# Kernel optimization log

Hardware: AMD Instinct MI355X
Metric: run time of the kernel (lower is better)

## Reference

```python
import jax, jax.numpy as jnp
import numpy as np

N = 100000      # nodes
E = 1600000     # edges
R = 4           # relations
F = 128         # node feature dim
EMB = 128       # embedding size
HID = 256       # hidden size
B = 1024        # number of (nest, food) queries


def setup_inputs() -> dict:
    key = jax.random.key(0)
    ks = jax.random.split(key, 12)
    s1 = 1.0 / np.sqrt(F)
    s2 = 1.0 / np.sqrt(EMB)
    sf = 1.0 / np.sqrt(2 * EMB)
    return {
        "x": jax.random.normal(ks[0], (N, F), jnp.float32),
        "edge_index": jax.random.randint(ks[1], (2, E), 0, N),
        "edge_type": jax.random.randint(ks[2], (E,), 0, R),
        "nest_idx": jax.random.randint(ks[3], (B,), 0, N),
        "food_idx": jax.random.randint(ks[4], (B,), 0, N),
        "W_rel1": jax.random.normal(ks[5], (R, F, EMB), jnp.float32) * s1,
        "W_root1": jax.random.normal(ks[6], (F, EMB), jnp.float32) * s1,
        "b1": jnp.zeros((EMB,), jnp.float32),
        "W_rel2": jax.random.normal(ks[7], (R, EMB, EMB), jnp.float32) * s2,
        "W_root2": jax.random.normal(ks[8], (EMB, EMB), jnp.float32) * s2,
        "b2": jnp.zeros((EMB,), jnp.float32),
        "W_fc": jax.random.normal(ks[9], (2 * EMB, HID), jnp.float32) * sf,
        "b_fc": jnp.zeros((HID,), jnp.float32),
    }


def rgcn_conv(x, src, dst, etype, W_rel, W_root, b):
    # Per-relation transform of all nodes: [N, R, O]
    h = jnp.einsum('nf,rfo->nro', x, W_rel)
    msgs = h[src, etype]                      # [E, O] gather per edge
    # Mean aggregation per (dst, relation), PyG RGCNConv default
    key = dst * R + etype                     # [E]
    deg = jax.ops.segment_sum(jnp.ones((E,), x.dtype), key, num_segments=N * R)
    norm = 1.0 / jnp.maximum(deg, 1.0)
    out = jax.ops.segment_sum(msgs * norm[key][:, None], dst, num_segments=N)
    return out + x @ W_root + b


def reference(x, edge_index, edge_type, nest_idx, food_idx,
              W_rel1, W_root1, b1, W_rel2, W_root2, b2, W_fc, b_fc):
    src, dst = edge_index[0], edge_index[1]
    h = jax.nn.relu(rgcn_conv(x, src, dst, edge_type, W_rel1, W_root1, b1))
    h = rgcn_conv(h, src, dst, edge_type, W_rel2, W_root2, b2)
    combined = jnp.concatenate([h[nest_idx], h[food_idx]], axis=-1)  # [B, 2*EMB]
    return jax.nn.relu(combined @ W_fc + b_fc)                        # [B, HID]
```

## Files before the change

### kernel.cpp

```cpp
#include <hip/hip_runtime.h>
#include <stdint.h>

#define NN 100000
#define NE 1600000
#define NR 4
#define FD 128
#define KA 512
#define KT 640
#define NQ 1024
#define HIDN 256

#define MPAD 100096
#define NBE ((NE + 2047) / 2048)
#define NCHB ((NN + 255) / 256)
#define MAXS 49152
#define NCH1 (MAXS / 256)
#define MAXL2 65536

using u16 = unsigned short;
using u32 = unsigned int;
using u8 = unsigned char;
typedef __attribute__((ext_vector_type(8))) __bf16 bf16x8;
typedef __attribute__((ext_vector_type(4))) float f32x4;

__device__ __forceinline__ u16 f2b(float f) {
    u32 u = __builtin_bit_cast(u32, f);
    u32 r = u + 0x7FFFu + ((u >> 16) & 1u);
    return (u16)(r >> 16);
}
__device__ __forceinline__ float b2f_lo(u32 v) { return __builtin_bit_cast(float, v << 16); }
__device__ __forceinline__ float b2f_hi(u32 v) { return __builtin_bit_cast(float, v & 0xFFFF0000u); }
__device__ __forceinline__ u32 pack2(float a, float b) {
    return (u32)f2b(a) | ((u32)f2b(b) << 16);
}
__device__ __forceinline__ void gload_lds16(const void* g, void* l) {
    __builtin_amdgcn_global_load_lds((const __attribute__((address_space(1))) u32*)g,
                                     (__attribute__((address_space(3))) u32*)l, 16, 0, 0);
}

__global__ __launch_bounds__(256) void mark_T(const int* __restrict__ nest,
                                              const int* __restrict__ food,
                                              u8* __restrict__ bmT, u8* __restrict__ bmS) {
    int i = blockIdx.x * 256 + threadIdx.x;
    if (i < NQ)          { int q = nest[i];      bmT[q] = 1; bmS[q] = 1; }
    else if (i < 2 * NQ) { int q = food[i - NQ]; bmT[q] = 1; bmS[q] = 1; }
}

__global__ __launch_bounds__(256) void filter_l2(const int* __restrict__ ei,
                                                 const int* __restrict__ et,
                                                 const u8* __restrict__ bmT,
                                                 u8* __restrict__ bmS,
                                                 int* __restrict__ cnts,
                                                 u32* __restrict__ l2a,
                                                 u32* __restrict__ l2d) {
    __shared__ int lcnt, lbase;
    __shared__ u32 ba[2048], bd[2048];
    int t = threadIdx.x;
    if (t == 0) lcnt = 0;
    __syncthreads();
    int e0 = blockIdx.x * 2048;
    for (int j = 0; j < 8; ++j) {
        int e = e0 + j * 256 + t;
        if (e < NE) {
            int dst = ei[NE + e];
            if (bmT[dst]) {
                int src = ei[e];
                int r = et[e];
                int pos = atomicAdd(&lcnt, 1);
                ba[pos] = (u32)src | ((u32)r << 17);
                bd[pos] = (u32)dst;
                bmS[src] = 1;
            }
        }
    }
    __syncthreads();
    if (t == 0) lbase = atomicAdd(&cnts[2], lcnt);
    __syncthreads();
    for (int i = t; i < lcnt; i += 256) {
        l2a[lbase + i] = ba[i];
        l2d[lbase + i] = bd[i];
    }
}

__global__ __launch_bounds__(256) void bm_chunk(const u8* __restrict__ bmS,
                                                const u8* __restrict__ bmT,
                                                int* __restrict__ cS, int* __restrict__ cT) {
    __shared__ int sS[256], sT[256];
    int b = blockIdx.x, t = threadIdx.x;
    int n = b * 256 + t;
    int vs = (n < NN) ? bmS[n] : 0;
    int vt = (n < NN) ? bmT[n] : 0;
    sS[t] = vs; sT[t] = vt;
    __syncthreads();
    for (int o = 128; o > 0; o >>= 1) {
        if (t < o) { sS[t] += sS[t + o]; sT[t] += sT[t + o]; }
        __syncthreads();
    }
    if (t == 0) { cS[b] = sS[0]; cT[b] = sT[0]; }
}

__global__ __launch_bounds__(512) void bm_scan(const int* __restrict__ cS,
                                               const int* __restrict__ cT,
                                               int* __restrict__ oS, int* __restrict__ oT,
                                               int* __restrict__ cnts) {
    __shared__ int sS[512], sT[512];
    int t = threadIdx.x;
    int vs = (t < NCHB) ? cS[t] : 0;
    int vt = (t < NCHB) ? cT[t] : 0;
    sS[t] = vs; sT[t] = vt;
    __syncthreads();
    for (int o = 1; o < 512; o <<= 1) {
        int a = (t >= o) ? sS[t - o] : 0;
        int c = (t >= o) ? sT[t - o] : 0;
        __syncthreads();
        sS[t] += a; sT[t] += c;
        __syncthreads();
    }
    if (t < NCHB) { oS[t] = sS[t] - vs; oT[t] = sT[t] - vt; }
    if (t == NCHB - 1) { cnts[0] = sS[t]; cnts[1] = sT[t]; }
}

__global__ __launch_bounds__(256) void bm_write(const u8* __restrict__ bmS,
                                                const u8* __restrict__ bmT,
                                                const int* __restrict__ oS,
                                                const int* __restrict__ oT,
                                                int* __restrict__ sid, int* __restrict__ tidm,
                                                int* __restrict__ snode) {
    __shared__ int sS[256], sT[256];
    int b = blockIdx.x, t = threadIdx.x;
    int n = b * 256 + t;
    int vs = (n < NN) ? bmS[n] : 0;
    int vt = (n < NN) ? bmT[n] : 0;
    sS[t] = vs; sT[t] = vt;
    __syncthreads();
    for (int o = 1; o < 256; o <<= 1) {
        int a = (t >= o) ? sS[t - o] : 0;
        int c = (t >= o) ? sT[t - o] : 0;
        __syncthreads();
        sS[t] += a; sT[t] += c;
        __syncthreads();
    }
    if (n < NN) {
        int is = oS[b] + sS[t] - vs;
        int it = oT[b] + sT[t] - vt;
        sid[n] = is;
        tidm[n] = it;
        if (vs) snode[is] = n;
    }
}

__global__ __launch_bounds__(256) void l2_count(const int* __restrict__ cnts,
                                                const u32* __restrict__ l2a,
                                                const u32* __restrict__ l2d,
                                                const int* __restrict__ tidm,
                                                int* __restrict__ deg2) {
    int n = cnts[2];
    for (int i = blockIdx.x * 256 + threadIdx.x; i < n; i += gridDim.x * 256)
        atomicAdd(&deg2[tidm[l2d[i]] * 4 + ((l2a[i] >> 17) & 3)], 1);
}

__global__ __launch_bounds__(1024) void l2_scan(const int* __restrict__ deg2,
                                                int* __restrict__ offs2,
                                                int* __restrict__ cur2) {
    __shared__ int sm[1024];
    int t = threadIdx.x;
    int v[8];
    int s = 0;
    for (int j = 0; j < 8; ++j) { v[j] = deg2[t * 8 + j]; s += v[j]; }
    sm[t] = s;
    __syncthreads();
    for (int o = 1; o < 1024; o <<= 1) {
        int n = (t >= o) ? sm[t - o] : 0;
        __syncthreads();
        sm[t] += n;
        __syncthreads();
    }
    int ex = sm[t] - s;
    for (int j = 0; j < 8; ++j) { offs2[t * 8 + j] = ex; cur2[t * 8 + j] = ex; ex += v[j]; }
    if (t == 1023) offs2[8192] = ex;
}

__global__ __launch_bounds__(256) void l2_scatter(const int* __restrict__ cnts,
                                                  const u32* __restrict__ l2a,
                                                  const u32* __restrict__ l2d,
                                                  const int* __restrict__ tidm,
                                                  const int* __restrict__ sid,
                                                  int* __restrict__ cur2,
                                                  int* __restrict__ spack2) {
    int n = cnts[2];
    for (int i = blockIdx.x * 256 + threadIdx.x; i < n; i += gridDim.x * 256) {
        u32 a = l2a[i];
        int k = tidm[l2d[i]] * 4 + ((a >> 17) & 3);
        int pos = atomicAdd(&cur2[k], 1);
        spack2[pos] = sid[a & 0x1FFFFu];
    }
}

__global__ __launch_bounds__(256) void l1_count(const int* __restrict__ ei,
                                                const int* __restrict__ et,
                                                const u8* __restrict__ bmS,
                                                const int* __restrict__ sid,
                                                int* __restrict__ deg1) {
    int e0 = blockIdx.x * 2048;
    int t = threadIdx.x;
    for (int j = 0; j < 8; ++j) {
        int e = e0 + j * 256 + t;
        if (e < NE) {
            int dst = ei[NE + e];
            if (bmS[dst]) atomicAdd(&deg1[sid[dst] * 4 + et[e]], 1);
        }
    }
}

__global__ __launch_bounds__(256) void l1_chunk(const int* __restrict__ deg1,
                                                int* __restrict__ c1) {
    __shared__ int sm[256];
    int b = blockIdx.x, t = threadIdx.x;
    int n = b * 256 + t;
    int s = deg1[4 * n] + deg1[4 * n + 1] + deg1[4 * n + 2] + deg1[4 * n + 3];
    sm[t] = (s + 7) & ~7;
    __syncthreads();
    for (int o = 128; o > 0; o >>= 1) {
        if (t < o) sm[t] += sm[t + o];
        __syncthreads();
    }
    if (t == 0) c1[b] = sm[0];
}

__global__ __launch_bounds__(256) void l1_scan(const int* __restrict__ c1,
                                               int* __restrict__ o1) {
    __shared__ int sm[256];
    int t = threadIdx.x;
    int v = (t < NCH1) ? c1[t] : 0;
    sm[t] = v;
    __syncthreads();
    for (int o = 1; o < 256; o <<= 1) {
        int n = (t >= o) ? sm[t - o] : 0;
        __syncthreads();
        sm[t] += n;
        __syncthreads();
    }
    if (t < NCH1) o1[t] = sm[t] - v;
}

__global__ __launch_bounds__(256) void l1_write(const int* __restrict__ deg1,
                                                const int* __restrict__ o1,
                                                int* __restrict__ offs6s,
                                                int* __restrict__ cur1,
                                                int* __restrict__ spack1) {
    __shared__ int sm[256];
    int b = blockIdx.x, t = threadIdx.x;
    int n = b * 256 + t;
    int d0 = deg1[4 * n], d1 = deg1[4 * n + 1], d2 = deg1[4 * n + 2], d3 = deg1[4 * n + 3];
    int s = d0 + d1 + d2 + d3;
    int sp = (s + 7) & ~7;
    sm[t] = sp;
    __syncthreads();
    for (int o = 1; o < 256; o <<= 1) {
        int v = (t >= o) ? sm[t - o] : 0;
        __syncthreads();
        sm[t] += v;
        __syncthreads();
    }
    int e0 = o1[b] + sm[t] - sp;
    int e1 = e0 + d0, e2 = e1 + d1, e3 = e2 + d2, e4 = e3 + d3, eL = e0 + sp;
    int* o6 = offs6s + (size_t)n * 6;
    o6[0] = e0; o6[1] = e1; o6[2] = e2; o6[3] = e3; o6[4] = e4; o6[5] = eL;
    cur1[4 * n] = e0; cur1[4 * n + 1] = e1; cur1[4 * n + 2] = e2; cur1[4 * n + 3] = e3;
    for (int i = e4; i < eL; ++i) spack1[i] = NN;
}

__global__ __launch_bounds__(256) void l1_scatter(const int* __restrict__ ei,
                                                  const int* __restrict__ et,
                                                  const u8* __restrict__ bmS,
                                                  const int* __restrict__ sid,
                                                  int* __restrict__ cur1,
                                                  int* __restrict__ spack1) {
    int e0 = blockIdx.x * 2048;
    int t = threadIdx.x;
    for (int j = 0; j < 8; ++j) {
        int e = e0 + j * 256 + t;
        if (e < NE) {
            int dst = ei[NE + e];
            if (bmS[dst]) {
                int pos = atomicAdd(&cur1[sid[dst] * 4 + et[e]], 1);
                spack1[pos] = ei[e];
            }
        }
    }
}

__global__ __launch_bounds__(256) void cvt_bf16(const float* __restrict__ in,
                                                u16* __restrict__ outp, int n) {
    int i = blockIdx.x * 256 + threadIdx.x;
    int idx = i * 4;
    if (idx >= n) return;
    float4 v = *(const float4*)(in + idx);
    u32 lo = (u32)f2b(v.x) | ((u32)f2b(v.y) << 16);
    u32 hi = (u32)f2b(v.z) | ((u32)f2b(v.w) << 16);
    *(uint2*)(outp + idx) = make_uint2(lo, hi);
}

__global__ __launch_bounds__(256) void prep_B(const float* __restrict__ Wrel,
                                              const float* __restrict__ Wroot,
                                              u16* __restrict__ Bt) {
    int i = blockIdx.x * 256 + threadIdx.x;
    if (i >= FD * KT) return;
    int k = i % KT;
    int o = i / KT;
    float v = (k < 512) ? Wrel[(size_t)k * FD + o] : Wroot[(size_t)(k - 512) * FD + o];
    Bt[i] = f2b(v);
}

__global__ __launch_bounds__(256) void agg_s(const int* __restrict__ cnts,
                                             const int* __restrict__ offs6s,
                                             const int* __restrict__ spack1,
                                             const u32* __restrict__ fp,
                                             u16* __restrict__ Aout) {
    int wid = threadIdx.x >> 6, lane = threadIdx.x & 63;
    int row = blockIdx.x * 4 + wid;
    if (row >= cnts[0]) return;

    const int* ob = offs6s + (size_t)row * 6;
    int o0 = __builtin_amdgcn_readfirstlane(ob[0]);
    int o1 = __builtin_amdgcn_readfirstlane(ob[1]);
    int o2 = __builtin_amdgcn_readfirstlane(ob[2]);
    int o3 = __builtin_amdgcn_readfirstlane(ob[3]);
    int o4 = __builtin_amdgcn_readfirstlane(ob[4]);
    int oL = __builtin_amdgcn_readfirstlane(ob[5]);

    float a00 = 0, a01 = 0, a10 = 0, a11 = 0, a20 = 0, a21 = 0, a30 = 0, a31 = 0;

    for (int e = o0; e < oL; e += 8) {
        int p[8];
        u32 v[8];
#pragma unroll
        for (int j = 0; j < 8; ++j)
            p[j] = __builtin_amdgcn_readfirstlane(spack1[e + j]);
#pragma unroll
        for (int j = 0; j < 8; ++j) v[j] = fp[(size_t)p[j] * 64 + lane];
#pragma unroll
        for (int j = 0; j < 8; ++j) {
            int ij = e + j;
            float f0 = b2f_lo(v[j]);
            float f1 = b2f_hi(v[j]);
            if (ij < o1)      { a00 += f0; a01 += f1; }
            else if (ij < o2) { a10 += f0; a11 += f1; }
            else if (ij < o3) { a20 += f0; a21 += f1; }
            else              { a30 += f0; a31 += f1; }
        }
    }

    int d0 = o1 - o0, d1 = o2 - o1, d2 = o3 - o2, d3 = o4 - o3;
    float s0 = 1.0f / (float)(d0 > 1 ? d0 : 1);
    float s1 = 1.0f / (float)(d1 > 1 ? d1 : 1);
    float s2 = 1.0f / (float)(d2 > 1 ? d2 : 1);
    float s3 = 1.0f / (float)(d3 > 1 ? d3 : 1);
    u16* Ao = Aout + (size_t)row * KA + lane * 2;
    __builtin_nontemporal_store(pack2(a00 * s0, a01 * s0), (u32*)(Ao + 0));
    __builtin_nontemporal_store(pack2(a10 * s1, a11 * s1), (u32*)(Ao + 128));
    __builtin_nontemporal_store(pack2(a20 * s2, a21 * s2), (u32*)(Ao + 256));
    __builtin_nontemporal_store(pack2(a30 * s3, a31 * s3), (u32*)(Ao + 384));
}

__global__ __launch_bounds__(256) void agg_q2(const int* __restrict__ offs2,
                                              const int* __restrict__ spack2,
                                              const u32* __restrict__ h1s4,
                                              const int* __restrict__ nest,
                                              const int* __restrict__ food,
                                              const int* __restrict__ tidm,
                                              const int* __restrict__ sid,
                                              u16* __restrict__ Aout,
                                              int* __restrict__ sidq) {
    int wid = threadIdx.x >> 6, lane = threadIdx.x & 63;
    int row = blockIdx.x * 4 + wid;
    if (row >= 2 * NQ) return;
    int q = (row < NQ) ? nest[row] : food[row - NQ];
    q = __builtin_amdgcn_readfirstlane(q);
    int tq = __builtin_amdgcn_readfirstlane(tidm[q]);
    if (lane == 0) sidq[row] = sid[q];
    const int* ob = offs2 + (size_t)tq * 4;
    int o[5];
#pragma unroll
    for (int i = 0; i < 5; ++i) o[i] = __builtin_amdgcn_readfirstlane(ob[i]);
    u16* Ao = Aout + (size_t)row * KA + lane * 2;
#pragma unroll
    for (int r = 0; r < 4; ++r) {
        int s = o[r], t = o[r + 1], last = t - 1;
        float a0 = 0, a1 = 0;
        for (int e = s; e < t; e += 8) {
            int p[8];
            u32 v[8];
#pragma unroll
            for (int j = 0; j < 8; ++j) {
                int ij = e + j;
                int cl = ij <= last ? ij : last;
                int pv = __builtin_amdgcn_readfirstlane(spack2[cl]);
                p[j] = (ij <= last) ? pv : MAXS;
            }
#pragma unroll
            for (int j = 0; j < 8; ++j) v[j] = h1s4[(size_t)p[j] * 64 + lane];
#pragma unroll
            for (int j = 0; j < 8; ++j) { a0 += b2f_lo(v[j]); a1 += b2f_hi(v[j]); }
        }
        int d = t - s;
        float sc = 1.0f / (float)(d > 1 ? d : 1);
        *(u32*)(Ao + r * 128) = pack2(a0 * sc, a1 * sc);
    }
}

__global__ __launch_bounds__(256) void gemm_lds3(const u16* __restrict__ A,
                                                 const u16* __restrict__ rootSrc,
                                                 const int* __restrict__ rootIdx,
                                                 const u16* __restrict__ Bt,
                                                 const float* __restrict__ bias,
                                                 void* __restrict__ Cout,
                                                 const int* __restrict__ Mptr, int Mstatic,
                                                 int relu, int outBf16) {
    int M = Mptr ? Mptr[0] : Mstatic;
    int row0 = blockIdx.x * 128;
    if (row0 >= M) return;
    __shared__ u16 As[3][8192];
    int tid = threadIdx.x;
    int wid = tid >> 6, lane = tid & 63;
    int wm = wid >> 1, wn = wid & 1;
    int lr = lane & 15, hi = lane >> 4;

    f32x4 acc[4][4];
#pragma unroll
    for (int i = 0; i < 4; ++i)
#pragma unroll
        for (int j = 0; j < 4; ++j) acc[i][j] = (f32x4){0.f, 0.f, 0.f, 0.f};

    int srow = wid * 8 + (lane >> 3);
    int sg = (lane & 7) ^ ((lane >> 3) & 7);

    auto stage = [&](int t, int buf) {
#pragma unroll
        for (int i = 0; i < 4; ++i) {
            int r = i * 32 + srow;
            int gr = row0 + r;
            const u16* src;
            if (t < 8) {
                src = A + (size_t)gr * KA + t * 64 + sg * 8;
            } else {
                int idx = rootIdx ? rootIdx[gr] : gr;
                if ((u32)idx > (u32)NN) idx = 0;
                src = rootSrc + (size_t)idx * FD + (t - 8) * 64 + sg * 8;
            }
            gload_lds16(src, (char*)As[buf] + i * 4096 + wid * 1024);
        }
    };

    stage(0, 0);
    stage(1, 1);

    for (int t = 0; t < 10; ++t) {
        int cur = t % 3;
        bf16x8 bfr[2][4];
#pragma unroll
        for (int kk = 0; kk < 2; ++kk)
#pragma unroll
            for (int ni = 0; ni < 4; ++ni) {
                int col = wn * 64 + ni * 16 + lr;
                bfr[kk][ni] = *reinterpret_cast<const bf16x8*>(
                    Bt + (size_t)col * KT + t * 64 + kk * 32 + hi * 8);
            }
        bool staged = (t + 2 < 10);
        if (staged) stage(t + 2, (t + 2) % 3);
        if (staged) asm volatile("s_waitcnt vmcnt(4)" ::: "memory");
        else        asm volatile("s_waitcnt vmcnt(0)" ::: "memory");
        __builtin_amdgcn_s_barrier();
        __builtin_amdgcn_sched_barrier(0);
#pragma unroll
        for (int kk = 0; kk < 2; ++kk) {
            bf16x8 afr[4];
#pragma unroll
            for (int mi = 0; mi < 4; ++mi) {
                int r = wm * 64 + mi * 16 + lr;
                int sp = (kk * 4 + hi) ^ (r & 7);
                afr[mi] = *reinterpret_cast<const bf16x8*>((char*)As[cur] + r * 128 + sp * 16);
            }
#pragma unroll
            for (int mi = 0; mi < 4; ++mi)
#pragma unroll
                for (int ni = 0; ni < 4; ++ni)
                    acc[mi][ni] = __builtin_amdgcn_mfma_f32_16x16x32_bf16(afr[mi], bfr[kk][ni], acc[mi][ni], 0, 0, 0);
        }
        asm volatile("s_waitcnt lgkmcnt(0)" ::: "memory");
        __builtin_amdgcn_s_barrier();
    }

#pragma unroll
    for (int mi = 0; mi < 4; ++mi)
#pragma unroll
        for (int ni = 0; ni < 4; ++ni) {
            int col = wn * 64 + ni * 16 + lr;
            float bv = bias[col];
#pragma unroll
            for (int rg = 0; rg < 4; ++rg) {
                int row = row0 + wm * 64 + mi * 16 + hi * 4 + rg;
                if (row < M) {
                    float v = acc[mi][ni][rg] + bv;
                    if (relu) v = fmaxf(v, 0.f);
                    if (outBf16) ((u16*)Cout)[(size_t)row * FD + col] = f2b(v);
                    else ((float*)Cout)[(size_t)row * FD + col] = v;
                }
            }
        }
}

__global__ __launch_bounds__(256) void fc_kernel(const float* __restrict__ h2q,
                                                 const float* __restrict__ Wfc,
                                                 const float* __restrict__ bfc,
                                                 float* __restrict__ out) {
    __shared__ float comb[2 * FD];
    int q = blockIdx.x, t = threadIdx.x;
    if (t < FD) comb[t] = h2q[(size_t)q * FD + t];
    else comb[t] = h2q[(size_t)(NQ + q) * FD + (t - FD)];
    __syncthreads();
    float s = bfc[t];
#pragma unroll 4
    for (int k = 0; k < 2 * FD; ++k) s += comb[k] * Wfc[(size_t)k * HIDN + t];
    out[(size_t)q * HIDN + t] = fmaxf(s, 0.f);
}

extern "C" void kernel_launch(void* const* d_in, const int* in_sizes, int n_in,
                              void* d_out, int out_size, void* d_ws, size_t ws_size,
                              hipStream_t stream) {
    const float* x      = (const float*)d_in[0];
    const int*   ei     = (const int*)d_in[1];
    const int*   et     = (const int*)d_in[2];
    const int*   nest   = (const int*)d_in[3];
    const int*   food   = (const int*)d_in[4];
    const float* Wrel1  = (const float*)d_in[5];
    const float* Wroot1 = (const float*)d_in[6];
    const float* b1     = (const float*)d_in[7];
    const float* Wrel2  = (const float*)d_in[8];
    const float* Wroot2 = (const float*)d_in[9];
    const float* b2     = (const float*)d_in[10];
    const float* Wfc    = (const float*)d_in[11];
    const float* bfc    = (const float*)d_in[12];
    float* out = (float*)d_out;

    char* w = (char*)d_ws;
    size_t off = 0;
    auto take = [&](size_t b) {
        char* p = w + off;
        off += b;
        off = (off + 255) & ~(size_t)255;
        return p;
    };
    size_t zero0 = off;
    int* cnts   = (int*)take(256);
    u8* bmT     = (u8*)take(NN);
    u8* bmS     = (u8*)take(NN);
    int* deg2   = (int*)take(8192 * 4);
    int* deg1   = (int*)take((size_t)4 * MAXS * 4);
    int* snode  = (int*)take((size_t)MAXS * 4);
    size_t zeroSz = off - zero0;
    char* zbase = w + zero0;
    int* oS     = (int*)take((size_t)NCHB * 4);
    int* oT     = (int*)take((size_t)NCHB * 4);
    int* c1     = (int*)take((size_t)NCH1 * 4);
    int* o1     = (int*)take((size_t)NCH1 * 4);
    int* sid    = (int*)take((size_t)NN * 4);
    int* tidm   = (int*)take((size_t)NN * 4);
    u32* l2a    = (u32*)take((size_t)MAXL2 * 4);
    u32* l2d    = (u32*)take((size_t)MAXL2 * 4);
    int* offs2  = (int*)take((size_t)8193 * 4);
    int* cur2   = (int*)take((size_t)8192 * 4);
    int* spack2 = (int*)take((size_t)MAXL2 * 4);
    int* offs6s = (int*)take((size_t)MAXS * 6 * 4);
    int* cur1   = (int*)take((size_t)4 * MAXS * 4);
    int* spack1 = (int*)take(((size_t)NE + 8 * MAXS) * 4);
    int* sidq   = (int*)take((size_t)2 * NQ * 4);
    u16* xh     = (u16*)take((size_t)MPAD * FD * 2);
    u16* Bt1    = (u16*)take((size_t)FD * KT * 2);
    u16* Bt2    = (u16*)take((size_t)FD * KT * 2);
    u16* A1s    = (u16*)take((size_t)MAXS * KA * 2);
    u16* h1s    = (u16*)take(((size_t)MAXS + 1) * FD * 2);
    u16* A2     = (u16*)take((size_t)2 * NQ * KA * 2);
    float* h2q  = (float*)take((size_t)2 * NQ * FD * 4);

    hipMemsetAsync(zbase, 0, zeroSz, stream);
    hipMemsetAsync(xh + (size_t)NN * FD, 0, FD * 2, stream);
    hipMemsetAsync(h1s + (size_t)MAXS * FD, 0, FD * 2, stream);

    cvt_bf16<<<((NN * FD / 4) + 255) / 256, 256, 0, stream>>>(x, xh, NN * FD);
    prep_B<<<(FD * KT + 255) / 256, 256, 0, stream>>>(Wrel1, Wroot1, Bt1);
    prep_B<<<(FD * KT + 255) / 256, 256, 0, stream>>>(Wrel2, Wroot2, Bt2);

    mark_T<<<(2 * NQ + 255) / 256, 256, 0, stream>>>(nest, food, bmT, bmS);
    filter_l2<<<NBE, 256, 0, stream>>>(ei, et, bmT, bmS, cnts, l2a, l2d);
    bm_chunk<<<NCHB, 256, 0, stream>>>(bmS, bmT, oS, oT);
    bm_scan<<<1, 512, 0, stream>>>(oS, oT, oS, oT, cnts);
    bm_write<<<NCHB, 256, 0, stream>>>(bmS, bmT, oS, oT, sid, tidm, snode);

    l2_count<<<128, 256, 0, stream>>>(cnts, l2a, l2d, tidm, deg2);
    l2_scan<<<1, 1024, 0, stream>>>(deg2, offs2, cur2);
    l2_scatter<<<128, 256, 0, stream>>>(cnts, l2a, l2d, tidm, sid, cur2, spack2);

    l1_count<<<NBE, 256, 0, stream>>>(ei, et, bmS, sid, deg1);
    l1_chunk<<<NCH1, 256, 0, stream>>>(deg1, c1);
    l1_scan<<<1, 256, 0, stream>>>(c1, o1);
    l1_write<<<NCH1, 256, 0, stream>>>(deg1, o1, offs6s, cur1, spack1);
    l1_scatter<<<NBE, 256, 0, stream>>>(ei, et, bmS, sid, cur1, spack1);

    agg_s<<<MAXS / 4, 256, 0, stream>>>(cnts, offs6s, spack1, (const u32*)xh, A1s);
    gemm_lds3<<<MAXS / 128, 256, 0, stream>>>(A1s, xh, snode, Bt1, b1,
                                              (void*)h1s, cnts, 0, 1, 1);

    agg_q2<<<(2 * NQ + 3) / 4, 256, 0, stream>>>(offs2, spack2, (const u32*)h1s,
                                                 nest, food, tidm, sid, A2, sidq);
    gemm_lds3<<<(2 * NQ) / 128, 256, 0, stream>>>(A2, h1s, sidq, Bt2, b2,
                                                  (void*)h2q, nullptr, 2 * NQ, 0, 0);
    fc_kernel<<<NQ, 256, 0, stream>>>(h2q, Wfc, bfc, out);
}
```

Measured before the change: 229.5 us.

## Replace scan-based compaction with atomic allocation and fuse prep kernels

Merges the bf16 conversion, the weight transposes and the query marking into one launch. It replaces the multi-kernel prefix-scan compactions (bitmap chunk/scan/write, the layer-2 count/scan and the layer-1 chunk/scan/write) with single-pass atomic-counter allocation. Layer-2 degrees are now counted directly in filter_l2 and indexed by node id, which drops the target-id map. This removes about eight kernel launches and their serial dependencies. In exchange the node order and CSR offsets become nondeterministic, and a larger per-node degree array (NN×4 ints) must be zeroed in the memset.

```diff
diff --git a/kernel.cpp b/kernel.cpp
--- a/kernel.cpp
+++ b/kernel.cpp
@@ -10,12 +10,12 @@
 #define NQ 1024
 #define HIDN 256
 
-#define MPAD 100096
 #define NBE ((NE + 2047) / 2048)
 #define NCHB ((NN + 255) / 256)
 #define MAXS 49152
 #define NCH1 (MAXS / 256)
 #define MAXL2 65536
+#define CVTB 12500
 
 using u16 = unsigned short;
 using u32 = unsigned int;
@@ -38,12 +38,43 @@
                                      (__attribute__((address_space(3))) u32*)l, 16, 0, 0);
 }
 
-__global__ __launch_bounds__(256) void mark_T(const int* __restrict__ nest,
-                                              const int* __restrict__ food,
-                                              u8* __restrict__ bmT, u8* __restrict__ bmS) {
-    int i = blockIdx.x * 256 + threadIdx.x;
-    if (i < NQ)          { int q = nest[i];      bmT[q] = 1; bmS[q] = 1; }
-    else if (i < 2 * NQ) { int q = food[i - NQ]; bmT[q] = 1; bmS[q] = 1; }
+__global__ __launch_bounds__(256) void prep_all(const float* __restrict__ x,
+                                                u16* __restrict__ xh,
+                                                const float* __restrict__ Wrel1,
+                                                const float* __restrict__ Wroot1,
+                                                u16* __restrict__ Bt1,
+                                                const float* __restrict__ Wrel2,
+                                                const float* __restrict__ Wroot2,
+                                                u16* __restrict__ Bt2,
+                                                const int* __restrict__ nest,
+                                                const int* __restrict__ food,
+                                                u8* __restrict__ bmT,
+                                                u8* __restrict__ bmS) {
+    int b = blockIdx.x, t = threadIdx.x;
+    if (b < CVTB) {
+        int idx = (b * 256 + t) * 4;
+        if (idx < NN * FD) {
+            float4 v = *(const float4*)(x + idx);
+            u32 lo = (u32)f2b(v.x) | ((u32)f2b(v.y) << 16);
+            u32 hi = (u32)f2b(v.z) | ((u32)f2b(v.w) << 16);
+            *(uint2*)(xh + idx) = make_uint2(lo, hi);
+        }
+    } else if (b < CVTB + 640) {
+        int rel2 = (b >= CVTB + 320);
+        int i = (b - CVTB - rel2 * 320) * 256 + t;
+        if (i < FD * KT) {
+            int k = i % KT;
+            int o = i / KT;
+            const float* Wr = rel2 ? Wrel2 : Wrel1;
+            const float* Wo = rel2 ? Wroot2 : Wroot1;
+            float v = (k < 512) ? Wr[(size_t)k * FD + o] : Wo[(size_t)(k - 512) * FD + o];
+            (rel2 ? Bt2 : Bt1)[i] = f2b(v);
+        }
+    } else {
+        int i = (b - CVTB - 640) * 256 + t;
+        if (i < NQ)          { int q = nest[i];      bmT[q] = 1; bmS[q] = 1; }
+        else if (i < 2 * NQ) { int q = food[i - NQ]; bmT[q] = 1; bmS[q] = 1; }
+    }
 }
 
 __global__ __launch_bounds__(256) void filter_l2(const int* __restrict__ ei,
@@ -51,6 +82,7 @@
                                                  const u8* __restrict__ bmT,
                                                  u8* __restrict__ bmS,
                                                  int* __restrict__ cnts,
+                                                 int* __restrict__ deg2n,
                                                  u32* __restrict__ l2a,
                                                  u32* __restrict__ l2d) {
     __shared__ int lcnt, lbase;
@@ -70,6 +102,7 @@
                 ba[pos] = (u32)src | ((u32)r << 17);
                 bd[pos] = (u32)dst;
                 bmS[src] = 1;
+                atomicAdd(&deg2n[dst * 4 + r], 1);
             }
         }
     }
@@ -82,116 +115,44 @@
     }
 }
 
-__global__ __launch_bounds__(256) void bm_chunk(const u8* __restrict__ bmS,
-                                                const u8* __restrict__ bmT,
-                                                int* __restrict__ cS, int* __restrict__ cT) {
-    __shared__ int sS[256], sT[256];
-    int b = blockIdx.x, t = threadIdx.x;
-    int n = b * 256 + t;
-    int vs = (n < NN) ? bmS[n] : 0;
-    int vt = (n < NN) ? bmT[n] : 0;
-    sS[t] = vs; sT[t] = vt;
-    __syncthreads();
-    for (int o = 128; o > 0; o >>= 1) {
-        if (t < o) { sS[t] += sS[t + o]; sT[t] += sT[t + o]; }
-        __syncthreads();
-    }
-    if (t == 0) { cS[b] = sS[0]; cT[b] = sT[0]; }
-}
-
-__global__ __launch_bounds__(512) void bm_scan(const int* __restrict__ cS,
-                                               const int* __restrict__ cT,
-                                               int* __restrict__ oS, int* __restrict__ oT,
-                                               int* __restrict__ cnts) {
-    __shared__ int sS[512], sT[512];
-    int t = threadIdx.x;
-    int vs = (t < NCHB) ? cS[t] : 0;
-    int vt = (t < NCHB) ? cT[t] : 0;
-    sS[t] = vs; sT[t] = vt;
-    __syncthreads();
-    for (int o = 1; o < 512; o <<= 1) {
-        int a = (t >= o) ? sS[t - o] : 0;
-        int c = (t >= o) ? sT[t - o] : 0;
-        __syncthreads();
-        sS[t] += a; sT[t] += c;
-        __syncthreads();
-    }
-    if (t < NCHB) { oS[t] = sS[t] - vs; oT[t] = sT[t] - vt; }
-    if (t == NCHB - 1) { cnts[0] = sS[t]; cnts[1] = sT[t]; }
-}
-
-__global__ __launch_bounds__(256) void bm_write(const u8* __restrict__ bmS,
-                                                const u8* __restrict__ bmT,
-                                                const int* __restrict__ oS,
-                                                const int* __restrict__ oT,
-                                                int* __restrict__ sid, int* __restrict__ tidm,
-                                                int* __restrict__ snode) {
-    __shared__ int sS[256], sT[256];
-    int b = blockIdx.x, t = threadIdx.x;
-    int n = b * 256 + t;
-    int vs = (n < NN) ? bmS[n] : 0;
-    int vt = (n < NN) ? bmT[n] : 0;
-    sS[t] = vs; sT[t] = vt;
-    __syncthreads();
-    for (int o = 1; o < 256; o <<= 1) {
-        int a = (t >= o) ? sS[t - o] : 0;
-        int c = (t >= o) ? sT[t - o] : 0;
-        __syncthreads();
-        sS[t] += a; sT[t] += c;
-        __syncthreads();
-    }
-    if (n < NN) {
-        int is = oS[b] + sS[t] - vs;
-        int it = oT[b] + sT[t] - vt;
+__global__ __launch_bounds__(256) void bm_compact(const u8* __restrict__ bmS,
+                                                  int* __restrict__ cnts,
+                                                  int* __restrict__ sid,
+                                                  int* __restrict__ snode) {
+    int n = blockIdx.x * 256 + threadIdx.x;
+    if (n < NN && bmS[n]) {
+        int is = atomicAdd(&cnts[0], 1);
         sid[n] = is;
-        tidm[n] = it;
-        if (vs) snode[is] = n;
-    }
-}
-
-__global__ __launch_bounds__(256) void l2_count(const int* __restrict__ cnts,
-                                                const u32* __restrict__ l2a,
-                                                const u32* __restrict__ l2d,
-                                                const int* __restrict__ tidm,
-                                                int* __restrict__ deg2) {
-    int n = cnts[2];
-    for (int i = blockIdx.x * 256 + threadIdx.x; i < n; i += gridDim.x * 256)
-        atomicAdd(&deg2[tidm[l2d[i]] * 4 + ((l2a[i] >> 17) & 3)], 1);
-}
-
-__global__ __launch_bounds__(1024) void l2_scan(const int* __restrict__ deg2,
-                                                int* __restrict__ offs2,
-                                                int* __restrict__ cur2) {
-    __shared__ int sm[1024];
-    int t = threadIdx.x;
-    int v[8];
-    int s = 0;
-    for (int j = 0; j < 8; ++j) { v[j] = deg2[t * 8 + j]; s += v[j]; }
-    sm[t] = s;
-    __syncthreads();
-    for (int o = 1; o < 1024; o <<= 1) {
-        int n = (t >= o) ? sm[t - o] : 0;
-        __syncthreads();
-        sm[t] += n;
-        __syncthreads();
-    }
-    int ex = sm[t] - s;
-    for (int j = 0; j < 8; ++j) { offs2[t * 8 + j] = ex; cur2[t * 8 + j] = ex; ex += v[j]; }
-    if (t == 1023) offs2[8192] = ex;
+        snode[is] = n;
+    }
+}
+
+__global__ __launch_bounds__(256) void l2_offs(const int* __restrict__ deg2n,
+                                               int* __restrict__ cnts,
+                                               int* __restrict__ offs2n,
+                                               int* __restrict__ cur2n) {
+    int n = blockIdx.x * 256 + threadIdx.x;
+    if (n >= NN) return;
+    int d0 = deg2n[n * 4], d1 = deg2n[n * 4 + 1], d2 = deg2n[n * 4 + 2], d3 = deg2n[n * 4 + 3];
+    int s = d0 + d1 + d2 + d3;
+    if (s == 0) return;
+    int base = atomicAdd(&cnts[3], s);
+    int e0 = base, e1 = e0 + d0, e2 = e1 + d1, e3 = e2 + d2;
+    offs2n[n * 4] = e0; offs2n[n * 4 + 1] = e1; offs2n[n * 4 + 2] = e2; offs2n[n * 4 + 3] = e3;
+    cur2n[n * 4] = e0;  cur2n[n * 4 + 1] = e1;  cur2n[n * 4 + 2] = e2;  cur2n[n * 4 + 3] = e3;
 }
 
 __global__ __launch_bounds__(256) void l2_scatter(const int* __restrict__ cnts,
                                                   const u32* __restrict__ l2a,
                                                   const u32* __restrict__ l2d,
-                                                  const int* __restrict__ tidm,
                                                   const int* __restrict__ sid,
-                                                  int* __restrict__ cur2,
+                                                  int* __restrict__ cur2n,
                                                   int* __restrict__ spack2) {
     int n = cnts[2];
     for (int i = blockIdx.x * 256 + threadIdx.x; i < n; i += gridDim.x * 256) {
         u32 a = l2a[i];
-        int k = tidm[l2d[i]] * 4 + ((a >> 17) & 3);
-        int pos = atomicAdd(&cur2[k], 1);
+        int k = (int)l2d[i] * 4 + (int)((a >> 17) & 3);
+        int pos = atomicAdd(&cur2n[k], 1);
         spack2[pos] = sid[a & 0x1FFFFu];
     }
 }
@@ -212,58 +173,18 @@
     }
 }
 
-__global__ __launch_bounds__(256) void l1_chunk(const int* __restrict__ deg1,
-                                                int* __restrict__ c1) {
-    __shared__ int sm[256];
-    int b = blockIdx.x, t = threadIdx.x;
-    int n = b * 256 + t;
-    int s = deg1[4 * n] + deg1[4 * n + 1] + deg1[4 * n + 2] + deg1[4 * n + 3];
-    sm[t] = (s + 7) & ~7;
-    __syncthreads();
-    for (int o = 128; o > 0; o >>= 1) {
-        if (t < o) sm[t] += sm[t + o];
-        __syncthreads();
-    }
-    if (t == 0) c1[b] = sm[0];
-}
-
-__global__ __launch_bounds__(256) void l1_scan(const int* __restrict__ c1,
-                                               int* __restrict__ o1) {
-    __shared__ int sm[256];
-    int t = threadIdx.x;
-    int v = (t < NCH1) ? c1[t] : 0;
-    sm[t] = v;
-    __syncthreads();
-    for (int o = 1; o < 256; o <<= 1) {
-        int n = (t >= o) ? sm[t - o] : 0;
-        __syncthreads();
-        sm[t] += n;
-        __syncthreads();
-    }
-    if (t < NCH1) o1[t] = sm[t] - v;
-}
-
-__global__ __launch_bounds__(256) void l1_write(const int* __restrict__ deg1,
-                                                const int* __restrict__ o1,
-                                                int* __restrict__ offs6s,
-                                                int* __restrict__ cur1,
-                                                int* __restrict__ spack1) {
-    __shared__ int sm[256];
-    int b = blockIdx.x, t = threadIdx.x;
-    int n = b * 256 + t;
+__global__ __launch_bounds__(256) void l1_offs(const int* __restrict__ deg1,
+                                               int* __restrict__ cnts,
+                                               int* __restrict__ offs6s,
+                                               int* __restrict__ cur1,
+                                               int* __restrict__ spack1) {
+    int n = blockIdx.x * 256 + threadIdx.x;
+    if (n >= MAXS) return;
     int d0 = deg1[4 * n], d1 = deg1[4 * n + 1], d2 = deg1[4 * n + 2], d3 = deg1[4 * n + 3];
     int s = d0 + d1 + d2 + d3;
     int sp = (s + 7) & ~7;
-    sm[t] = sp;
-    __syncthreads();
-    for (int o = 1; o < 256; o <<= 1) {
-        int v = (t >= o) ? sm[t - o] : 0;
-        __syncthreads();
-        sm[t] += v;
-        __syncthreads();
-    }
-    int e0 = o1[b] + sm[t] - sp;
-    int e1 = e0 + d0, e2 = e1 + d1, e3 = e2 + d2, e4 = e3 + d3, eL = e0 + sp;
+    int base = sp ? atomicAdd(&cnts[4], sp) : 0;
+    int e0 = base, e1 = e0 + d0, e2 = e1 + d1, e3 = e2 + d2, e4 = e3 + d3, eL = base + sp;
     int* o6 = offs6s + (size_t)n * 6;
     o6[0] = e0; o6[1] = e1; o6[2] = e2; o6[3] = e3; o6[4] = e4; o6[5] = eL;
     cur1[4 * n] = e0; cur1[4 * n + 1] = e1; cur1[4 * n + 2] = e2; cur1[4 * n + 3] = e3;
@@ -290,28 +211,6 @@
     }
 }
 
-__global__ __launch_bounds__(256) void cvt_bf16(const float* __restrict__ in,
-                                                u16* __restrict__ outp, int n) {
-    int i = blockIdx.x * 256 + threadIdx.x;
-    int idx = i * 4;
-    if (idx >= n) return;
-    float4 v = *(const float4*)(in + idx);
-    u32 lo = (u32)f2b(v.x) | ((u32)f2b(v.y) << 16);
-    u32 hi = (u32)f2b(v.z) | ((u32)f2b(v.w) << 16);
-    *(uint2*)(outp + idx) = make_uint2(lo, hi);
-}
-
-__global__ __launch_bounds__(256) void prep_B(const float* __restrict__ Wrel,
-                                              const float* __restrict__ Wroot,
-                                              u16* __restrict__ Bt) {
-    int i = blockIdx.x * 256 + threadIdx.x;
-    if (i >= FD * KT) return;
-    int k = i % KT;
-    int o = i / KT;
-    float v = (k < 512) ? Wrel[(size_t)k * FD + o] : Wroot[(size_t)(k - 512) * FD + o];
-    Bt[i] = f2b(v);
-}
-
 __global__ __launch_bounds__(256) void agg_s(const int* __restrict__ cnts,
                                              const int* __restrict__ offs6s,
                                              const int* __restrict__ spack1,
@@ -363,12 +262,12 @@
     __builtin_nontemporal_store(pack2(a30 * s3, a31 * s3), (u32*)(Ao + 384));
 }
 
-__global__ __launch_bounds__(256) void agg_q2(const int* __restrict__ offs2,
+__global__ __launch_bounds__(256) void agg_q2(const int* __restrict__ offs2n,
+                                              const int* __restrict__ deg2n,
                                               const int* __restrict__ spack2,
                                               const u32* __restrict__ h1s4,
                                               const int* __restrict__ nest,
                                               const int* __restrict__ food,
-                                              const int* __restrict__ tidm,
                                               const int* __restrict__ sid,
                                               u16* __restrict__ Aout,
                                               int* __restrict__ sidq) {
@@ -377,16 +276,13 @@
     if (row >= 2 * NQ) return;
     int q = (row < NQ) ? nest[row] : food[row - NQ];
     q = __builtin_amdgcn_readfirstlane(q);
-    int tq = __builtin_amdgcn_readfirstlane(tidm[q]);
     if (lane == 0) sidq[row] = sid[q];
-    const int* ob = offs2 + (size_t)tq * 4;
-    int o[5];
-#pragma unroll
-    for (int i = 0; i < 5; ++i) o[i] = __builtin_amdgcn_readfirstlane(ob[i]);
     u16* Ao = Aout + (size_t)row * KA + lane * 2;
 #pragma unroll
     for (int r = 0; r < 4; ++r) {
-        int s = o[r], t = o[r + 1], last = t - 1;
+        int s = __builtin_amdgcn_readfirstlane(offs2n[q * 4 + r]);
+        int d = __builtin_amdgcn_readfirstlane(deg2n[q * 4 + r]);
+        int t = s + d, last = t - 1;
         float a0 = 0, a1 = 0;
         for (int e = s; e < t; e += 8) {
             int p[8];
@@ -403,7 +299,6 @@
 #pragma unroll
             for (int j = 0; j < 8; ++j) { a0 += b2f_lo(v[j]); a1 += b2f_hi(v[j]); }
         }
-        int d = t - s;
         float sc = 1.0f / (float)(d > 1 ? d : 1);
         *(u32*)(Ao + r * 128) = pack2(a0 * sc, a1 * sc);
     }
@@ -551,68 +446,52 @@
         off = (off + 255) & ~(size_t)255;
         return p;
     };
+    u16* xh     = (u16*)take((size_t)NN * FD * 2);
     size_t zero0 = off;
+    take(FD * 2);
     int* cnts   = (int*)take(256);
     u8* bmT     = (u8*)take(NN);
     u8* bmS     = (u8*)take(NN);
-    int* deg2   = (int*)take(8192 * 4);
+    int* deg2n  = (int*)take((size_t)NN * 4 * 4);
     int* deg1   = (int*)take((size_t)4 * MAXS * 4);
     int* snode  = (int*)take((size_t)MAXS * 4);
+    u16* h1s    = (u16*)take(((size_t)MAXS + 1) * FD * 2);
     size_t zeroSz = off - zero0;
     char* zbase = w + zero0;
-    int* oS     = (int*)take((size_t)NCHB * 4);
-    int* oT     = (int*)take((size_t)NCHB * 4);
-    int* c1     = (int*)take((size_t)NCH1 * 4);
-    int* o1     = (int*)take((size_t)NCH1 * 4);
     int* sid    = (int*)take((size_t)NN * 4);
-    int* tidm   = (int*)take((size_t)NN * 4);
     u32* l2a    = (u32*)take((size_t)MAXL2 * 4);
     u32* l2d    = (u32*)take((size_t)MAXL2 * 4);
-    int* offs2  = (int*)take((size_t)8193 * 4);
-    int* cur2   = (int*)take((size_t)8192 * 4);
+    int* offs2n = (int*)take((size_t)NN * 4 * 4);
+    int* cur2n  = (int*)take((size_t)NN * 4 * 4);
     int* spack2 = (int*)take((size_t)MAXL2 * 4);
     int* offs6s = (int*)take((size_t)MAXS * 6 * 4);
     int* cur1   = (int*)take((size_t)4 * MAXS * 4);
     int* spack1 = (int*)take(((size_t)NE + 8 * MAXS) * 4);
     int* sidq   = (int*)take((size_t)2 * NQ * 4);
-    u16* xh     = (u16*)take((size_t)MPAD * FD * 2);
     u16* Bt1    = (u16*)take((size_t)FD * KT * 2);
     u16* Bt2    = (u16*)take((size_t)FD * KT * 2);
     u16* A1s    = (u16*)take((size_t)MAXS * KA * 2);
-    u16* h1s    = (u16*)take(((size_t)MAXS + 1) * FD * 2);
     u16* A2     = (u16*)take((size_t)2 * NQ * KA * 2);
     float* h2q  = (float*)take((size_t)2 * NQ * FD * 4);
 
     hipMemsetAsync(zbase, 0, zeroSz, stream);
-    hipMemsetAsync(xh + (size_t)NN * FD, 0, FD * 2, stream);
-    hipMemsetAsync(h1s + (size_t)MAXS * FD, 0, FD * 2, stream);
-
-    cvt_bf16<<<((NN * FD / 4) + 255) / 256, 256, 0, stream>>>(x, xh, NN * FD);
-    prep_B<<<(FD * KT + 255) / 256, 256, 0, stream>>>(Wrel1, Wroot1, Bt1);
-    prep_B<<<(FD * KT + 255) / 256, 256, 0, stream>>>(Wrel2, Wroot2, Bt2);
-
-    mark_T<<<(2 * NQ + 255) / 256, 256, 0, stream>>>(nest, food, bmT, bmS);
-    filter_l2<<<NBE, 256, 0, stream>>>(ei, et, bmT, bmS, cnts, l2a, l2d);
-    bm_chunk<<<NCHB, 256, 0, stream>>>(bmS, bmT, oS, oT);
-    bm_scan<<<1, 512, 0, stream>>>(oS, oT, oS, oT, cnts);
-    bm_write<<<NCHB, 256, 0, stream>>>(bmS, bmT, oS, oT, sid, tidm, snode);
-
-    l2_count<<<128, 256, 0, stream>>>(cnts, l2a, l2d, tidm, deg2);
-    l2_scan<<<1, 1024, 0, stream>>>(deg2, offs2, cur2);
-    l2_scatter<<<128, 256, 0, stream>>>(cnts, l2a, l2d, tidm, sid, cur2, spack2);
-
+
+    prep_all<<<CVTB + 640 + 8, 256, 0, stream>>>(x, xh, Wrel1, Wroot1, Bt1,
+                                                 Wrel2, Wroot2, Bt2, nest, food, bmT, bmS);
+    filter_l2<<<NBE, 256, 0, stream>>>(ei, et, bmT, bmS, cnts, deg2n, l2a, l2d);
+    bm_compact<<<NCHB, 256, 0, stream>>>(bmS, cnts, sid, snode);
+    l2_offs<<<NCHB, 256, 0, stream>>>(deg2n, cnts, offs2n, cur2n);
+    l2_scatter<<<128, 256, 0, stream>>>(cnts, l2a, l2d, sid, cur2n, spack2);
     l1_count<<<NBE, 256, 0, stream>>>(ei, et, bmS, sid, deg1);
-    l1_chunk<<<NCH1, 256, 0, stream>>>(deg1, c1);
-    l1_scan<<<1, 256, 0, stream>>>(c1, o1);
-    l1_write<<<NCH1, 256, 0, stream>>>(deg1, o1, offs6s, cur1, spack1);
+    l1_offs<<<NCH1, 256, 0, stream>>>(deg1, cnts, offs6s, cur1, spack1);
     l1_scatter<<<NBE, 256, 0, stream>>>(ei, et, bmS, sid, cur1, spack1);
 
     agg_s<<<MAXS / 4, 256, 0, stream>>>(cnts, offs6s, spack1, (const u32*)xh, A1s);
     gemm_lds3<<<MAXS / 128, 256, 0, stream>>>(A1s, xh, snode, Bt1, b1,
                                               (void*)h1s, cnts, 0, 1, 1);
 
-    agg_q2<<<(2 * NQ + 3) / 4, 256, 0, stream>>>(offs2, spack2, (const u32*)h1s,
-                                                 nest, food, tidm, sid, A2, sidq);
+    agg_q2<<<(2 * NQ + 3) / 4, 256, 0, stream>>>(offs2n, deg2n, spack2, (const u32*)h1s,
+                                                 nest, food, sid, A2, sidq);
     gemm_lds3<<<(2 * NQ) / 128, 256, 0, stream>>>(A2, h1s, sidq, Bt2, b2,
                                                   (void*)h2q, nullptr, 2 * NQ, 0, 0);
     fc_kernel<<<NQ, 256, 0, stream>>>(h2q, Wfc, bfc, out);
```

Measured after the change: 243.8 us. 6.2% more time.
